# Kernel optimization log

Measured on AMD Instinct MI355X. Metric: run time of the kernel, lower is better.

Reference implementation:

```python
import jax, jax.numpy as jnp
import numpy as np

O, T, DIN, H, DOUT = 50000, 500000, 128, 256, 128


def setup_inputs() -> dict:
    key = jax.random.key(0)
    ks = jax.random.split(key, 12)
    s = 0.05
    return {
        "obj_vecs": jax.random.normal(ks[0], (O, DIN), jnp.float32),
        "pred_vecs": jax.random.normal(ks[1], (T, DIN), jnp.float32),
        "edges": jax.random.randint(ks[2], (T, 2), 0, O, jnp.int64),
        "w1a": jax.random.normal(ks[3], (3 * DIN, H), jnp.float32) * s,
        "b1a": jax.random.normal(ks[4], (H,), jnp.float32) * s,
        "w1b": jax.random.normal(ks[5], (H, 2 * H + DOUT), jnp.float32) * s,
        "b1b": jax.random.normal(ks[6], (2 * H + DOUT,), jnp.float32) * s,
        "w2a": jax.random.normal(ks[7], (H, H), jnp.float32) * s,
        "b2a": jax.random.normal(ks[8], (H,), jnp.float32) * s,
        "w2b": jax.random.normal(ks[9], (H, DOUT), jnp.float32) * s,
        "b2b": jax.random.normal(ks[10], (DOUT,), jnp.float32) * s,
    }


def reference(obj_vecs, pred_vecs, edges, w1a, b1a, w1b, b1b, w2a, b2a, w2b, b2b):
    n_obj = obj_vecs.shape[0]
    h_dim = w2a.shape[0]
    d_out = w2b.shape[1]
    s_idx = edges[:, 0]
    o_idx = edges[:, 1]
    # gather subject/object node features, concat with predicate: [T, 3*Din]
    cur_t = jnp.concatenate([obj_vecs[s_idx], pred_vecs, obj_vecs[o_idx]], axis=1)
    # edge MLP (net1): Linear-ReLU-Linear-ReLU -> [T, 2H + Dout]
    new_t = jax.nn.relu(jax.nn.relu(cur_t @ w1a + b1a) @ w1b + b1b)
    new_s = new_t[:, :h_dim]
    new_p = new_t[:, h_dim:h_dim + d_out]
    new_o = new_t[:, h_dim + d_out:]
    # scatter-add pooling back to nodes, both endpoints
    idx = jnp.concatenate([s_idx, o_idx])
    vals = jnp.concatenate([new_s, new_o], axis=0)
    pooled = jax.ops.segment_sum(vals, idx, num_segments=n_obj)
    # avg pooling: divide by per-node incidence count (clamped to >= 1)
    counts = jax.ops.segment_sum(jnp.ones(idx.shape[0], obj_vecs.dtype), idx,
                                 num_segments=n_obj)
    pooled = pooled / jnp.clip(counts, 1.0)[:, None]
    # node MLP (net2)
    new_obj = jax.nn.relu(jax.nn.relu(pooled @ w2a + b2a) @ w2b + b2b)
    return new_obj, new_p
```

## Files before the change

kernel.cpp:

```cpp
#include <hip/hip_runtime.h>


using f32x4 = __attribute__((ext_vector_type(4))) float;
using s16x8 = __attribute__((ext_vector_type(8))) short;
typedef unsigned short u16x8 __attribute__((ext_vector_type(8)));

static __device__ __forceinline__ unsigned short f2b(float f) {
    unsigned int u = __float_as_uint(f);
    unsigned int r = (u + 0x7fffu + ((u >> 16) & 1u)) >> 16;
    return (unsigned short)r;
}

static __device__ __forceinline__ float b2f(unsigned short b) {
    return __uint_as_float(((unsigned)b) << 16);
}

static __device__ __forceinline__ unsigned swz(unsigned row, unsigned byteoff) {
    return byteoff ^ ((row & 7u) << 4);
}

static __device__ __forceinline__ void gload_lds16(const unsigned short* g, unsigned short* l) {
    __builtin_amdgcn_global_load_lds(
        (const __attribute__((address_space(1))) unsigned int*)g,
        (__attribute__((address_space(3))) unsigned int*)l,
        16, 0, 0);
}

__global__ void prep_weights(const float* __restrict__ w1a, const float* __restrict__ w1b,
                             const float* __restrict__ w2a, const float* __restrict__ w2b,
                             unsigned short* __restrict__ w1aT, unsigned short* __restrict__ w1bT,
                             unsigned short* __restrict__ w2aT, unsigned short* __restrict__ w2bT) {
    int t = blockIdx.x * blockDim.x + threadIdx.x;
    if (t < 2 * 6 * 8192) {
        int tile = t >> 13; int nc1 = tile / 6, kt = tile % 6;
        int rem = t & 8191; int c = rem >> 6, kk = rem & 63;
        unsigned byte = ((unsigned)(c * 128 + kk * 2)) ^ ((c & 7u) << 4);
        *(unsigned short*)((char*)w1aT + (size_t)tile * 16384 + byte) =
            f2b(w1a[(size_t)(kt * 64 + kk) * 256 + nc1 * 128 + c]);
        return;
    }
    t -= 98304;
    if (t < 5 * 4 * 8192) {
        int tile = t >> 13; int nc = tile >> 2, kt2 = tile & 3;
        int rem = t & 8191; int c = rem >> 6, kk = rem & 63;
        unsigned byte = ((unsigned)(c * 128 + kk * 2)) ^ ((c & 7u) << 4);
        *(unsigned short*)((char*)w1bT + (size_t)tile * 16384 + byte) =
            f2b(w1b[(size_t)(kt2 * 64 + kk) * 640 + nc * 128 + c]);
        return;
    }
    t -= 163840;
    if (t < 65536) { int n = t >> 8, k = t & 255; w2aT[t] = f2b(w2a[k * 256 + n]); return; }
    t -= 65536;
    if (t < 32768) { int n = t >> 8, k = t & 255; w2bT[t] = f2b(w2b[k * 128 + n]); return; }
}

__global__ void count_kernel_i(const int* __restrict__ edges, int* __restrict__ cnt, int T) {
    int e = blockIdx.x * blockDim.x + threadIdx.x;
    if (e < T) {
        atomicAdd(&cnt[edges[2 * (long long)e]], 1);
        atomicAdd(&cnt[edges[2 * (long long)e + 1]], 1);
    }
}

__global__ void scan_kernel(const int* __restrict__ cnt, int* __restrict__ rowptr,
                            int* __restrict__ cursor, int O) {
    __shared__ int sc[1024];
    const int tid = threadIdx.x;
    const int per = (O + 1023) >> 10;
    const int base = tid * per;
    int s = 0;
    for (int i = 0; i < per; ++i) { int j = base + i; if (j < O) s += cnt[j]; }
    sc[tid] = s;
    __syncthreads();
    for (int d = 1; d < 1024; d <<= 1) {
        int v = (tid >= d) ? sc[tid - d] : 0;
        __syncthreads();
        sc[tid] += v;
        __syncthreads();
    }
    int off = sc[tid] - s;
    for (int i = 0; i < per; ++i) {
        int j = base + i;
        if (j < O) { rowptr[j] = off; cursor[j] = off; off += cnt[j]; }
    }
    if (tid == 0) rowptr[O] = sc[1023];
}

__global__ void fill_kernel(const int* __restrict__ edges, int* __restrict__ cursor,
                            int* __restrict__ csr, int T) {
    int e = blockIdx.x * blockDim.x + threadIdx.x;
    if (e < T) {
        int s = edges[2 * (long long)e];
        int o = edges[2 * (long long)e + 1];
        int ps = atomicAdd(&cursor[s], 1); csr[ps] = e;
        int po = atomicAdd(&cursor[o], 1); csr[po] = T + e;
    }
}

__global__ __launch_bounds__(256, 3) void edge_mlp(
    const float* __restrict__ obj, const float* __restrict__ pred,
    const int* __restrict__ edges,
    const unsigned short* __restrict__ w1aT, const float* __restrict__ b1a,
    const unsigned short* __restrict__ w1bT, const float* __restrict__ b1b,
    unsigned short* __restrict__ edgeout, float* __restrict__ outP, int T) {
    const int m0 = blockIdx.x * 64;
    const int tid = threadIdx.x;
    const int lane = tid & 63, wid = tid >> 6;
    const int wm = wid >> 1, wn = wid & 1;
    const bool evenL = ((lane & 1) == 0);

    __shared__ unsigned short Hbuf[64 * 256];
    __shared__ unsigned short Bbuf[8192];
    unsigned short* Abuf = Hbuf;

    bool okR[2][4];
    #pragma unroll
    for (int mi = 0; mi < 2; ++mi)
        #pragma unroll
        for (int rr = 0; rr < 4; ++rr)
            okR[mi][rr] = (m0 + wm * 32 + mi * 16 + ((lane >> 4) << 2) + rr) < T;

    const int r = tid >> 2;
    const int q = tid & 3;
    int e_r = m0 + r; if (e_r >= T) e_r = T - 1;
    const int sIdx_r = edges[2 * (long long)e_r];
    const int oIdx_r = edges[2 * (long long)e_r + 1];

    f32x4 acc1[2][2][4];
    #pragma unroll
    for (int a = 0; a < 2; ++a)
        #pragma unroll
        for (int b = 0; b < 2; ++b)
            #pragma unroll
            for (int c = 0; c < 4; ++c) acc1[a][b][c] = f32x4{0.f, 0.f, 0.f, 0.f};

    for (int kt = 0; kt < 6; ++kt) {
        {
            const float* src;
            if (kt < 2)      src = obj  + (long long)sIdx_r * 128 + kt * 64;
            else if (kt < 4) src = pred + (long long)e_r   * 128 + (kt - 2) * 64;
            else             src = obj  + (long long)oIdx_r * 128 + (kt - 4) * 64;
            const float4* s4 = (const float4*)src;
            #pragma unroll
            for (int i = 0; i < 4; ++i) {
                float4 v = s4[q * 4 + i];
                ushort4 pk; pk.x = f2b(v.x); pk.y = f2b(v.y); pk.z = f2b(v.z); pk.w = f2b(v.w);
                unsigned byte = (r * 128u + q * 32u + i * 8u) ^ ((r & 7u) << 4);
                *(ushort4*)((char*)Abuf + byte) = pk;
            }
        }
        #pragma unroll
        for (int nc1 = 0; nc1 < 2; ++nc1) {
            const unsigned short* gt = w1aT + (size_t)(nc1 * 6 + kt) * 8192;
            #pragma unroll
            for (int rr4 = 0; rr4 < 4; ++rr4) {
                unsigned off = wid * 4096u + rr4 * 1024u;
                gload_lds16((const unsigned short*)((const char*)gt + off + lane * 16u),
                            (unsigned short*)((char*)Bbuf + off));
            }
            __syncthreads();
            #pragma unroll
            for (int ks = 0; ks < 2; ++ks) {
                const unsigned kk = ks * 32u + ((lane >> 4) << 3);
                s16x8 af[2];
                #pragma unroll
                for (int mi = 0; mi < 2; ++mi) {
                    unsigned row = wm * 32u + mi * 16u + (lane & 15);
                    af[mi] = *(const s16x8*)((const char*)Abuf + ((row * 128u + kk * 2u) ^ ((row & 7u) << 4)));
                }
                #pragma unroll
                for (int nj = 0; nj < 4; ++nj) {
                    unsigned c = wn * 64u + nj * 16u + (lane & 15);
                    s16x8 bf = *(const s16x8*)((const char*)Bbuf + ((c * 128u + kk * 2u) ^ ((c & 7u) << 4)));
                    #pragma unroll
                    for (int mi = 0; mi < 2; ++mi)
                        acc1[nc1][mi][nj] = __builtin_amdgcn_mfma_f32_16x16x32_bf16(af[mi], bf, acc1[nc1][mi][nj], 0, 0, 0);
                }
            }
            __syncthreads();
        }
    }

    #pragma unroll
    for (int nb = 0; nb < 2; ++nb)
        #pragma unroll
        for (int nj = 0; nj < 4; ++nj) {
            int col = nb * 128 + wn * 64 + nj * 16 + (lane & 15);
            float bias = b1a[col];
            #pragma unroll
            for (int mi = 0; mi < 2; ++mi)
                #pragma unroll
                for (int rr = 0; rr < 4; ++rr) {
                    unsigned row = wm * 32u + mi * 16u + ((lane >> 4) << 2) + rr;
                    float v = acc1[nb][mi][nj][rr] + bias;
                    v = v > 0.f ? v : 0.f;
                    *(unsigned short*)((char*)Hbuf + swz(row, row * 512u + col * 2u)) = f2b(v);
                }
        }
    __syncthreads();

    #pragma unroll
    for (int nc = 0; nc < 5; ++nc) {
        f32x4 acc2[2][4];
        #pragma unroll
        for (int b = 0; b < 2; ++b)
            #pragma unroll
            for (int c = 0; c < 4; ++c) acc2[b][c] = f32x4{0.f, 0.f, 0.f, 0.f};

        #pragma unroll
        for (int kt2 = 0; kt2 < 4; ++kt2) {
            const unsigned short* gt = w1bT + (size_t)(nc * 4 + kt2) * 8192;
            #pragma unroll
            for (int rr4 = 0; rr4 < 4; ++rr4) {
                unsigned off = wid * 4096u + rr4 * 1024u;
                gload_lds16((const unsigned short*)((const char*)gt + off + lane * 16u),
                            (unsigned short*)((char*)Bbuf + off));
            }
            __syncthreads();
            #pragma unroll
            for (int ks = 0; ks < 2; ++ks) {
                const unsigned kkB = ks * 32u + ((lane >> 4) << 3);
                const unsigned kkH = kt2 * 64u + kkB;
                s16x8 af[2];
                #pragma unroll
                for (int mi = 0; mi < 2; ++mi) {
                    unsigned row = wm * 32u + mi * 16u + (lane & 15);
                    af[mi] = *(const s16x8*)((const char*)Hbuf + swz(row, row * 512u + kkH * 2u));
                }
                #pragma unroll
                for (int nj = 0; nj < 4; ++nj) {
                    unsigned c = wn * 64u + nj * 16u + (lane & 15);
                    s16x8 bf = *(const s16x8*)((const char*)Bbuf + ((c * 128u + kkB * 2u) ^ ((c & 7u) << 4)));
                    #pragma unroll
                    for (int mi = 0; mi < 2; ++mi)
                        acc2[mi][nj] = __builtin_amdgcn_mfma_f32_16x16x32_bf16(af[mi], bf, acc2[mi][nj], 0, 0, 0);
                }
            }
            __syncthreads();
        }

        if (nc == 2) {
            #pragma unroll
            for (int nj = 0; nj < 4; ++nj) {
                int col = nc * 128 + wn * 64 + nj * 16 + (lane & 15);
                float bias = b1b[col];
                #pragma unroll
                for (int mi = 0; mi < 2; ++mi)
                    #pragma unroll
                    for (int rr = 0; rr < 4; ++rr) {
                        int row = wm * 32 + mi * 16 + ((lane >> 4) << 2) + rr;
                        if (okR[mi][rr]) {
                            float v = acc2[mi][nj][rr] + bias;
                            v = v > 0.f ? v : 0.f;
                            outP[(long long)(m0 + row) * 128 + (col - 256)] = v;
                        }
                    }
            }
        } else {
            #pragma unroll
            for (int nj = 0; nj < 4; ++nj) {
                int col = nc * 128 + wn * 64 + nj * 16 + (lane & 15);
                float bias = b1b[col];
                int pc = (nc < 2) ? col : (col - 384);
                int pcb = (lane & 1) ? (pc - 1) : pc;
                #pragma unroll
                for (int mi = 0; mi < 2; ++mi) {
                    float vv[4];
                    #pragma unroll
                    for (int rr = 0; rr < 4; ++rr) {
                        float v = acc2[mi][nj][rr] + bias;
                        vv[rr] = v > 0.f ? v : 0.f;
                    }
                    float nb0 = __shfl_xor(vv[0], 1);
                    float nb1 = __shfl_xor(vv[1], 1);
                    float nb2 = __shfl_xor(vv[2], 1);
                    float nb3 = __shfl_xor(vv[3], 1);
                    #pragma unroll
                    for (int k = 0; k < 2; ++k) {
                        float lo = evenL ? (k ? vv[1] : vv[0]) : (k ? nb3 : nb2);
                        float hi = evenL ? (k ? nb1 : nb0) : (k ? vv[3] : vv[2]);
                        int rsel = evenL ? k : 2 + k;
                        if (okR[mi][rsel]) {
                            int row = wm * 32 + mi * 16 + ((lane >> 4) << 2) + rsel;
                            size_t e = (size_t)(m0 + row);
                            size_t rid = (nc < 2) ? e : (size_t)T + e;
                            unsigned pk = ((unsigned)f2b(hi) << 16) | f2b(lo);
                            *(unsigned*)(edgeout + rid * 256 + pcb) = pk;
                        }
                    }
                }
            }
        }
    }
}

__global__ __launch_bounds__(256, 4) void pool_gather(
    const unsigned short* __restrict__ edgeout, const int* __restrict__ rowptr,
    const int* __restrict__ csr, unsigned short* __restrict__ pooled, int O) {
    int w = blockIdx.x * 4 + (threadIdx.x >> 6);
    if (w >= O) return;
    const int lane = threadIdx.x & 63;
    const int beg = rowptr[w], end = rowptr[w + 1];
    float ax = 0.f, ay = 0.f, az = 0.f, aw = 0.f;
    float bx = 0.f, by = 0.f, bz = 0.f, bw = 0.f;
    int i = beg;
    for (; i + 1 < end; i += 2) {
        int r0 = csr[i], r1 = csr[i + 1];
        ushort4 v0 = *(const ushort4*)(edgeout + (size_t)r0 * 256 + lane * 4);
        ushort4 v1 = *(const ushort4*)(edgeout + (size_t)r1 * 256 + lane * 4);
        ax += b2f(v0.x); ay += b2f(v0.y); az += b2f(v0.z); aw += b2f(v0.w);
        bx += b2f(v1.x); by += b2f(v1.y); bz += b2f(v1.z); bw += b2f(v1.w);
    }
    if (i < end) {
        int r0 = csr[i];
        ushort4 v0 = *(const ushort4*)(edgeout + (size_t)r0 * 256 + lane * 4);
        ax += b2f(v0.x); ay += b2f(v0.y); az += b2f(v0.z); aw += b2f(v0.w);
    }
    float inv = 1.f / fmaxf((float)(end - beg), 1.f);
    ushort4 o4;
    o4.x = f2b((ax + bx) * inv); o4.y = f2b((ay + by) * inv);
    o4.z = f2b((az + bz) * inv); o4.w = f2b((aw + bw) * inv);
    *(ushort4*)(pooled + (size_t)w * 256 + lane * 4) = o4;
}

__global__ __launch_bounds__(256, 2) void obj_mlp(
    const unsigned short* __restrict__ pooled,
    const unsigned short* __restrict__ w2aT, const float* __restrict__ b2a,
    const unsigned short* __restrict__ w2bT, const float* __restrict__ b2b,
    float* __restrict__ outObj, int O) {
    const int m0 = blockIdx.x * 64;
    const int tid = threadIdx.x;
    const int lane = tid & 63, wid = tid >> 6;
    const int wm = wid >> 1, wn = wid & 1;

    __shared__ unsigned short Abuf[64 * 256];

    {
        const int r = tid >> 2, q = tid & 3;
        int objc = m0 + r; if (objc >= O) objc = O - 1;
        const u16x8* s8 = (const u16x8*)(pooled + (size_t)objc * 256);
        #pragma unroll
        for (int i = 0; i < 8; ++i) {
            u16x8 v = s8[q * 8 + i];
            unsigned byte = r * 512u + (q * 64u + i * 8u) * 2u;
            *(u16x8*)((char*)Abuf + swz(r, byte)) = v;
        }
    }
    __syncthreads();

    f32x4 acc1[2][2][4];
    #pragma unroll
    for (int a = 0; a < 2; ++a)
        #pragma unroll
        for (int b = 0; b < 2; ++b)
            #pragma unroll
            for (int c = 0; c < 4; ++c) acc1[a][b][c] = f32x4{0.f, 0.f, 0.f, 0.f};
    #pragma unroll
    for (int ks = 0; ks < 8; ++ks) {
        const int klane = ks * 32 + ((lane >> 4) << 3);
        s16x8 af[2];
        #pragma unroll
        for (int mi = 0; mi < 2; ++mi) {
            int row = wm * 32 + mi * 16 + (lane & 15);
            af[mi] = *(const s16x8*)((const char*)Abuf + swz(row, row * 512u + klane * 2u));
        }
        #pragma unroll
        for (int nb = 0; nb < 2; ++nb)
            #pragma unroll
            for (int nj = 0; nj < 4; ++nj) {
                int col = nb * 128 + wn * 64 + nj * 16 + (lane & 15);
                s16x8 bf = *(const s16x8*)(w2aT + (long long)col * 256 + klane);
                #pragma unroll
                for (int mi = 0; mi < 2; ++mi)
                    acc1[nb][mi][nj] = __builtin_amdgcn_mfma_f32_16x16x32_bf16(af[mi], bf, acc1[nb][mi][nj], 0, 0, 0);
            }
    }
    __syncthreads();

    #pragma unroll
    for (int nb = 0; nb < 2; ++nb)
        #pragma unroll
        for (int nj = 0; nj < 4; ++nj) {
            int col = nb * 128 + wn * 64 + nj * 16 + (lane & 15);
            float bias = b2a[col];
            #pragma unroll
            for (int mi = 0; mi < 2; ++mi)
                #pragma unroll
                for (int rr = 0; rr < 4; ++rr) {
                    int row = wm * 32 + mi * 16 + ((lane >> 4) << 2) + rr;
                    float v = acc1[nb][mi][nj][rr] + bias;
                    v = v > 0.f ? v : 0.f;
                    *(unsigned short*)((char*)Abuf + swz(row, row * 512u + col * 2u)) = f2b(v);
                }
        }
    __syncthreads();

    f32x4 acc2[2][4];
    #pragma unroll
    for (int b = 0; b < 2; ++b)
        #pragma unroll
        for (int c = 0; c < 4; ++c) acc2[b][c] = f32x4{0.f, 0.f, 0.f, 0.f};
    #pragma unroll
    for (int ks = 0; ks < 8; ++ks) {
        const int klane = ks * 32 + ((lane >> 4) << 3);
        s16x8 af[2];
        #pragma unroll
        for (int mi = 0; mi < 2; ++mi) {
            int row = wm * 32 + mi * 16 + (lane & 15);
            af[mi] = *(const s16x8*)((const char*)Abuf + swz(row, row * 512u + klane * 2u));
        }
        #pragma unroll
        for (int nj = 0; nj < 4; ++nj) {
            int col = wn * 64 + nj * 16 + (lane & 15);
            s16x8 bf = *(const s16x8*)(w2bT + (long long)col * 256 + klane);
            #pragma unroll
            for (int mi = 0; mi < 2; ++mi)
                acc2[mi][nj] = __builtin_amdgcn_mfma_f32_16x16x32_bf16(af[mi], bf, acc2[mi][nj], 0, 0, 0);
        }
    }

    #pragma unroll
    for (int nj = 0; nj < 4; ++nj) {
        int col = wn * 64 + nj * 16 + (lane & 15);
        float bias = b2b[col];
        #pragma unroll
        for (int mi = 0; mi < 2; ++mi)
            #pragma unroll
            for (int rr = 0; rr < 4; ++rr) {
                int row = wm * 32 + mi * 16 + ((lane >> 4) << 2) + rr;
                int o = m0 + row;
                if (o < O) {
                    float v = acc2[mi][nj][rr] + bias;
                    v = v > 0.f ? v : 0.f;
                    outObj[(long long)o * 128 + col] = v;
                }
            }
    }
}

extern "C" void kernel_launch(void* const* d_in, const int* in_sizes, int n_in,
                              void* d_out, int out_size, void* d_ws, size_t ws_size,
                              hipStream_t stream) {
    const float* obj  = (const float*)d_in[0];
    const float* pred = (const float*)d_in[1];
    const int*   edges = (const int*)d_in[2];
    const float* w1a = (const float*)d_in[3];
    const float* b1a = (const float*)d_in[4];
    const float* w1b = (const float*)d_in[5];
    const float* b1b = (const float*)d_in[6];
    const float* w2a = (const float*)d_in[7];
    const float* b2a = (const float*)d_in[8];
    const float* w2b = (const float*)d_in[9];
    const float* b2b = (const float*)d_in[10];

    const int O = in_sizes[0] / 128;
    const int T = in_sizes[1] / 128;

    auto al = [](size_t x) { return (x + 255) & ~(size_t)255; };
    const size_t szEdgeout = (size_t)2 * T * 256 * 2;
    const size_t szPooled  = (size_t)O * 256 * 2;
    const size_t szCnt     = (size_t)O * 4;
    const size_t szRow     = (size_t)(O + 1) * 4;
    const size_t szCsr     = (size_t)2 * T * 4;

    size_t off = 0;
    char* ws = (char*)d_ws;
    unsigned short* edgeout = (unsigned short*)(ws + off); off += al(szEdgeout);
    unsigned short* pooled  = (unsigned short*)(ws + off); off += al(szPooled);
    int* cnt    = (int*)(ws + off); off += al(szCnt);
    int* cursor = (int*)(ws + off); off += al(szCnt);
    int* rowptr = (int*)(ws + off); off += al(szRow);
    int* csr    = (int*)(ws + off); off += al(szCsr);
    unsigned short* w1aT = (unsigned short*)(ws + off); off += (size_t)12 * 8192 * 2;
    unsigned short* w1bT = (unsigned short*)(ws + off); off += (size_t)20 * 8192 * 2;
    unsigned short* w2aT = (unsigned short*)(ws + off); off += (size_t)256 * 256 * 2;
    unsigned short* w2bT = (unsigned short*)(ws + off);

    float* outObj = (float*)d_out;
    float* outP   = (float*)d_out + (size_t)O * 128;

    hipMemsetAsync(cnt, 0, szCnt, stream);
    const int prepElems = 98304 + 163840 + 65536 + 32768;
    prep_weights<<<(prepElems + 255) / 256, 256, 0, stream>>>(w1a, w1b, w2a, w2b, w1aT, w1bT, w2aT, w2bT);
    count_kernel_i<<<(T + 255) / 256, 256, 0, stream>>>(edges, cnt, T);
    scan_kernel<<<1, 1024, 0, stream>>>(cnt, rowptr, cursor, O);
    fill_kernel<<<(T + 255) / 256, 256, 0, stream>>>(edges, cursor, csr, T);
    edge_mlp<<<(T + 63) / 64, 256, 0, stream>>>(obj, pred, edges, w1aT, b1a, w1bT, b1b, edgeout, outP, T);
    pool_gather<<<(O + 3) / 4, 256, 0, stream>>>(edgeout, rowptr, csr, pooled, O);
    obj_mlp<<<(O + 63) / 64, 256, 0, stream>>>(pooled, w2aT, b2a, w2bT, b2b, outObj, O);
}
```

Before: 956.6 us.

## Double-buffer A and B LDS tiles in edge MLP to overlap loads with MFMA

Splits LDS into two A buffers and two B buffers so the next weight tile (via global_load_lds) and the next gathered activation tile are fetched while MFMAs run on the current ones. This also removes one barrier per tile in both GEMM phases. The goal is to hide global-load latency that the single-buffered version exposed. Larger LDS use (64KB) forces launch bounds down from 3 to 2 blocks per CU, trading occupancy for software pipelining.

```diff
diff --git a/kernel.cpp b/kernel.cpp
--- a/kernel.cpp
+++ b/kernel.cpp
@@ -97,7 +97,7 @@
     }
 }
 
-__global__ __launch_bounds__(256, 3) void edge_mlp(
+__global__ __launch_bounds__(256, 2) void edge_mlp(
     const float* __restrict__ obj, const float* __restrict__ pred,
     const int* __restrict__ edges,
     const unsigned short* __restrict__ w1aT, const float* __restrict__ b1a,
@@ -109,9 +109,13 @@
     const int wm = wid >> 1, wn = wid & 1;
     const bool evenL = ((lane & 1) == 0);
 
-    __shared__ unsigned short Hbuf[64 * 256];
-    __shared__ unsigned short Bbuf[8192];
-    unsigned short* Abuf = Hbuf;
+    __shared__ unsigned short U[32768];
+    char* const ldsb = (char*)U;
+    unsigned short* const abuf0 = (unsigned short*)(ldsb);
+    unsigned short* const abuf1 = (unsigned short*)(ldsb + 8192);
+    unsigned short* const Hbuf  = (unsigned short*)(ldsb);
+    unsigned short* const bbuf0 = (unsigned short*)(ldsb + 32768);
+    unsigned short* const bbuf1 = (unsigned short*)(ldsb + 49152);
 
     bool okR[2][4];
     #pragma unroll
@@ -126,6 +130,33 @@
     const int sIdx_r = edges[2 * (long long)e_r];
     const int oIdx_r = edges[2 * (long long)e_r + 1];
 
+    auto aSrc = [&](int kt) -> const float4* {
+        const float* s;
+        if (kt < 2)      s = obj  + (long long)sIdx_r * 128 + kt * 64;
+        else if (kt < 4) s = pred + (long long)e_r   * 128 + (kt - 2) * 64;
+        else             s = obj  + (long long)oIdx_r * 128 + (kt - 4) * 64;
+        return (const float4*)s;
+    };
+
+    auto stageB = [&](const unsigned short* gt, unsigned short* bb) {
+        #pragma unroll
+        for (int rr4 = 0; rr4 < 4; ++rr4) {
+            unsigned off = wid * 4096u + rr4 * 1024u;
+            gload_lds16((const unsigned short*)((const char*)gt + off + lane * 16u),
+                        (unsigned short*)((char*)bb + off));
+        }
+    };
+
+    auto writeA = [&](const float4* ap, unsigned short* ab) {
+        #pragma unroll
+        for (int i = 0; i < 4; ++i) {
+            float4 v = ap[i];
+            ushort4 pk; pk.x = f2b(v.x); pk.y = f2b(v.y); pk.z = f2b(v.z); pk.w = f2b(v.w);
+            unsigned byte = (r * 128u + q * 32u + i * 8u) ^ ((r & 7u) << 4);
+            *(ushort4*)((char*)ab + byte) = pk;
+        }
+    };
+
     f32x4 acc1[2][2][4];
     #pragma unroll
     for (int a = 0; a < 2; ++a)
@@ -134,53 +165,55 @@
             #pragma unroll
             for (int c = 0; c < 4; ++c) acc1[a][b][c] = f32x4{0.f, 0.f, 0.f, 0.f};
 
+    auto mfma1 = [&](const unsigned short* ab, const unsigned short* bb, int nc1) {
+        #pragma unroll
+        for (int ks = 0; ks < 2; ++ks) {
+            const unsigned kk = ks * 32u + ((lane >> 4) << 3);
+            s16x8 af[2];
+            #pragma unroll
+            for (int mi = 0; mi < 2; ++mi) {
+                unsigned row = wm * 32u + mi * 16u + (lane & 15);
+                af[mi] = *(const s16x8*)((const char*)ab + ((row * 128u + kk * 2u) ^ ((row & 7u) << 4)));
+            }
+            #pragma unroll
+            for (int nj = 0; nj < 4; ++nj) {
+                unsigned c = wn * 64u + nj * 16u + (lane & 15);
+                s16x8 bf = *(const s16x8*)((const char*)bb + ((c * 128u + kk * 2u) ^ ((c & 7u) << 4)));
+                #pragma unroll
+                for (int mi = 0; mi < 2; ++mi)
+                    acc1[nc1][mi][nj] = __builtin_amdgcn_mfma_f32_16x16x32_bf16(af[mi], bf, acc1[nc1][mi][nj], 0, 0, 0);
+            }
+        }
+    };
+
+    float4 ap[4];
+    {
+        const float4* s4 = aSrc(0);
+        #pragma unroll
+        for (int i = 0; i < 4; ++i) ap[i] = s4[q * 4 + i];
+    }
+    stageB(w1aT + (size_t)(0 * 6 + 0) * 8192, bbuf0);
+    writeA(ap, abuf0);
+    __syncthreads();
+
+    #pragma unroll
     for (int kt = 0; kt < 6; ++kt) {
-        {
-            const float* src;
-            if (kt < 2)      src = obj  + (long long)sIdx_r * 128 + kt * 64;
-            else if (kt < 4) src = pred + (long long)e_r   * 128 + (kt - 2) * 64;
-            else             src = obj  + (long long)oIdx_r * 128 + (kt - 4) * 64;
-            const float4* s4 = (const float4*)src;
-            #pragma unroll
-            for (int i = 0; i < 4; ++i) {
-                float4 v = s4[q * 4 + i];
-                ushort4 pk; pk.x = f2b(v.x); pk.y = f2b(v.y); pk.z = f2b(v.z); pk.w = f2b(v.w);
-                unsigned byte = (r * 128u + q * 32u + i * 8u) ^ ((r & 7u) << 4);
-                *(ushort4*)((char*)Abuf + byte) = pk;
-            }
-        }
-        #pragma unroll
-        for (int nc1 = 0; nc1 < 2; ++nc1) {
-            const unsigned short* gt = w1aT + (size_t)(nc1 * 6 + kt) * 8192;
-            #pragma unroll
-            for (int rr4 = 0; rr4 < 4; ++rr4) {
-                unsigned off = wid * 4096u + rr4 * 1024u;
-                gload_lds16((const unsigned short*)((const char*)gt + off + lane * 16u),
-                            (unsigned short*)((char*)Bbuf + off));
-            }
-            __syncthreads();
-            #pragma unroll
-            for (int ks = 0; ks < 2; ++ks) {
-                const unsigned kk = ks * 32u + ((lane >> 4) << 3);
-                s16x8 af[2];
-                #pragma unroll
-                for (int mi = 0; mi < 2; ++mi) {
-                    unsigned row = wm * 32u + mi * 16u + (lane & 15);
-                    af[mi] = *(const s16x8*)((const char*)Abuf + ((row * 128u + kk * 2u) ^ ((row & 7u) << 4)));
-                }
-                #pragma unroll
-                for (int nj = 0; nj < 4; ++nj) {
-                    unsigned c = wn * 64u + nj * 16u + (lane & 15);
-                    s16x8 bf = *(const s16x8*)((const char*)Bbuf + ((c * 128u + kk * 2u) ^ ((c & 7u) << 4)));
-                    #pragma unroll
-                    for (int mi = 0; mi < 2; ++mi)
-                        acc1[nc1][mi][nj] = __builtin_amdgcn_mfma_f32_16x16x32_bf16(af[mi], bf, acc1[nc1][mi][nj], 0, 0, 0);
-                }
-            }
-            __syncthreads();
-        }
-    }
-
+        unsigned short* const ab = (kt & 1) ? abuf1 : abuf0;
+        stageB(w1aT + (size_t)(1 * 6 + kt) * 8192, bbuf1);
+        if (kt < 5) {
+            const float4* s4 = aSrc(kt + 1);
+            #pragma unroll
+            for (int i = 0; i < 4; ++i) ap[i] = s4[q * 4 + i];
+        }
+        mfma1(ab, bbuf0, 0);
+        __syncthreads();
+        if (kt < 5) stageB(w1aT + (size_t)(0 * 6 + (kt + 1)) * 8192, bbuf0);
+        mfma1(ab, bbuf1, 1);
+        if (kt < 5) writeA(ap, (kt & 1) ? abuf0 : abuf1);
+        __syncthreads();
+    }
+
+    stageB(w1bT, bbuf0);
     #pragma unroll
     for (int nb = 0; nb < 2; ++nb)
         #pragma unroll
@@ -209,14 +242,9 @@
 
         #pragma unroll
         for (int kt2 = 0; kt2 < 4; ++kt2) {
-            const unsigned short* gt = w1bT + (size_t)(nc * 4 + kt2) * 8192;
-            #pragma unroll
-            for (int rr4 = 0; rr4 < 4; ++rr4) {
-                unsigned off = wid * 4096u + rr4 * 1024u;
-                gload_lds16((const unsigned short*)((const char*)gt + off + lane * 16u),
-                            (unsigned short*)((char*)Bbuf + off));
-            }
-            __syncthreads();
+            if (kt2 < 3)           stageB(w1bT + (size_t)(nc * 4 + kt2 + 1) * 8192, (kt2 & 1) ? bbuf0 : bbuf1);
+            else if (nc < 4)       stageB(w1bT + (size_t)((nc + 1) * 4) * 8192, bbuf0);
+            unsigned short* const bb = (kt2 & 1) ? bbuf1 : bbuf0;
             #pragma unroll
             for (int ks = 0; ks < 2; ++ks) {
                 const unsigned kkB = ks * 32u + ((lane >> 4) << 3);
@@ -230,7 +258,7 @@
                 #pragma unroll
                 for (int nj = 0; nj < 4; ++nj) {
                     unsigned c = wn * 64u + nj * 16u + (lane & 15);
-                    s16x8 bf = *(const s16x8*)((const char*)Bbuf + ((c * 128u + kkB * 2u) ^ ((c & 7u) << 4)));
+                    s16x8 bf = *(const s16x8*)((const char*)bb + ((c * 128u + kkB * 2u) ^ ((c & 7u) << 4)));
                     #pragma unroll
                     for (int mi = 0; mi < 2; ++mi)
                         acc2[mi][nj] = __builtin_amdgcn_mfma_f32_16x16x32_bf16(af[mi], bf, acc2[mi][nj], 0, 0, 0);
```

Measured after the change: 1.017 ms. 6.3% more time.
